# Kernel tuning notes

Measured on AMD Instinct MI355X. Metric: run time of the kernel, lower is better.

Reference implementation:

```python
import jax, jax.numpy as jnp
import numpy as np

B, N, RIN, ROUT, DEMB, FIN, FE, E, ITERS = 64, 128, 32, 64, 64, 64, 16, 65536, 3
NTOT = B * N


def gnn(x, edge_index, edge_feat, Ws, Wm, We, b):
    # edge-conditioned message passing: [NTOT, Fin] -> [NTOT, Fout]
    src, dst = edge_index[0], edge_index[1]
    msg = jax.nn.relu(x[src] @ Wm + edge_feat @ We)          # [E, Fout]
    agg = jax.ops.segment_sum(msg, dst, num_segments=x.shape[0])
    return jax.nn.relu(x @ Ws + agg + b)


def setup_inputs() -> dict:
    key = jax.random.key(0)
    ks = jax.random.split(key, 20)
    s = 0.1
    return {
        "x_r": jax.random.normal(ks[0], (NTOT, FIN), jnp.float32),
        "edge_index_r": jax.random.randint(ks[1], (2, E), 0, NTOT),
        "edge_feat_r": jax.random.normal(ks[2], (E, FE), jnp.float32),
        "x_p": jax.random.normal(ks[3], (NTOT, FIN), jnp.float32),
        "edge_index_p": jax.random.randint(ks[4], (2, E), 0, NTOT),
        "edge_feat_p": jax.random.normal(ks[5], (E, FE), jnp.float32),
        "r_mask": jnp.ones((B, N), dtype=bool),
        "p_mask": jnp.ones((B, N), dtype=bool),
        # gnn_1 params (FIN -> DEMB)
        "g1_Ws": jax.random.normal(ks[6], (FIN, DEMB)) * s,
        "g1_Wm": jax.random.normal(ks[7], (FIN, DEMB)) * s,
        "g1_We": jax.random.normal(ks[8], (FE, DEMB)) * s,
        "g1_b": jnp.zeros((DEMB,), jnp.float32),
        # gnn_2 params (RIN -> ROUT)
        "g2_Ws": jax.random.normal(ks[9], (RIN, ROUT)) * s,
        "g2_Wm": jax.random.normal(ks[10], (RIN, ROUT)) * s,
        "g2_We": jax.random.normal(ks[11], (FE, ROUT)) * s,
        "g2_b": jnp.zeros((ROUT,), jnp.float32),
        # consensus mlp (ROUT -> ROUT -> 1)
        "mlp_W1": jax.random.normal(ks[12], (ROUT, ROUT)) * s,
        "mlp_b1": jnp.zeros((ROUT,), jnp.float32),
        "mlp_W2": jax.random.normal(ks[13], (ROUT, 1)) * s,
        "mlp_b2": jnp.zeros((1,), jnp.float32),
    }


def reference(x_r, edge_index_r, edge_feat_r, x_p, edge_index_p, edge_feat_p,
              r_mask, p_mask,
              g1_Ws, g1_Wm, g1_We, g1_b,
              g2_Ws, g2_Wm, g2_We, g2_b,
              mlp_W1, mlp_b1, mlp_W2, mlp_b2):
    # node embeddings via gnn_1, then dense-batch to [B, N, DEMB]
    h_r = gnn(x_r, edge_index_r, edge_feat_r, g1_Ws, g1_Wm, g1_We, g1_b).reshape(B, N, DEMB)
    h_p = gnn(x_p, edge_index_p, edge_feat_p, g1_Ws, g1_Wm, g1_We, g1_b).reshape(B, N, DEMB)

    M_hat = jnp.einsum('brd,bpd->brp', h_r, h_p)             # [B, N_r, N_p]
    M_mask = r_mask[:, :, None] & p_mask[:, None, :]
    M_0 = jax.nn.softmax(M_hat, axis=-1).reshape(NTOT, N)    # packed (full mask)

    rkey = jax.random.key(42)
    for it in range(ITERS):
        M = jax.nn.softmax(M_hat, axis=-1)
        rf_r = jax.random.normal(jax.random.fold_in(rkey, it), (B, N, RIN), jnp.float32)
        rf_p = jnp.einsum('brp,bri->bpi', M, rf_r)           # M^T @ rand
        o_r = gnn(rf_r.reshape(NTOT, RIN), edge_index_r, edge_feat_r,
                  g2_Ws, g2_Wm, g2_We, g2_b).reshape(B, N, ROUT)
        o_p = gnn(rf_p.reshape(NTOT, RIN), edge_index_p, edge_feat_p,
                  g2_Ws, g2_Wm, g2_We, g2_b).reshape(B, N, ROUT)
        D = o_r[:, :, None, :] - o_p[:, None, :, :]          # [B, N_r, N_p, ROUT]
        upd = (jax.nn.relu(D @ mlp_W1 + mlp_b1) @ mlp_W2 + mlp_b2)[..., 0]
        M_hat = M_hat + jnp.where(M_mask, upd, 0.0)

    M_T = jax.nn.softmax(M_hat, axis=-1).reshape(NTOT, N)
    return (M_0, M_T)
```

## Files before the change

### kernel.cpp

```cpp
#include <hip/hip_runtime.h>

constexpr int kE = 65536, kNTOT = 8192;

__host__ __device__ __forceinline__ void tf_round(unsigned& x0, unsigned& x1, int r) {
  x0 += x1;
  x1 = (x1 << r) | (x1 >> (32 - r));
  x1 ^= x0;
}
__host__ __device__ __forceinline__ void tf2x32(unsigned k0, unsigned k1,
                                                unsigned& x0, unsigned& x1) {
  unsigned ks2 = k0 ^ k1 ^ 0x1BD11BDAu;
  x0 += k0; x1 += k1;
  tf_round(x0,x1,13); tf_round(x0,x1,15); tf_round(x0,x1,26); tf_round(x0,x1,6);
  x0 += k1; x1 += ks2 + 1u;
  tf_round(x0,x1,17); tf_round(x0,x1,29); tf_round(x0,x1,16); tf_round(x0,x1,24);
  x0 += ks2; x1 += k0 + 2u;
  tf_round(x0,x1,13); tf_round(x0,x1,15); tf_round(x0,x1,26); tf_round(x0,x1,6);
  x0 += k0; x1 += k1 + 3u;
  tf_round(x0,x1,17); tf_round(x0,x1,29); tf_round(x0,x1,16); tf_round(x0,x1,24);
  x0 += k1; x1 += ks2 + 4u;
  tf_round(x0,x1,13); tf_round(x0,x1,15); tf_round(x0,x1,26); tf_round(x0,x1,6);
  x0 += ks2; x1 += k0 + 5u;
}

__device__ __forceinline__ float bits_to_normal(unsigned bits) {
  float f = __uint_as_float((bits >> 9) | 0x3f800000u) - 1.0f;
  const float LO = -0.99999994f;
  float u = fmaf(f, 2.0f, LO);
  u = fmaxf(u, LO);
  float w = -log1pf(-u * u);
  float p;
  if (w < 5.0f) {
    w -= 2.5f;
    p = 2.81022636e-08f;
    p = fmaf(p, w, 3.43273939e-07f);
    p = fmaf(p, w, -3.5233877e-06f);
    p = fmaf(p, w, -4.39150654e-06f);
    p = fmaf(p, w, 0.00021858087f);
    p = fmaf(p, w, -0.00125372503f);
    p = fmaf(p, w, -0.00417768164f);
    p = fmaf(p, w, 0.246640727f);
    p = fmaf(p, w, 1.50140941f);
  } else {
    w = sqrtf(w) - 3.0f;
    p = -0.000200214257f;
    p = fmaf(p, w, 0.000100950558f);
    p = fmaf(p, w, 0.00134934322f);
    p = fmaf(p, w, -0.00367342844f);
    p = fmaf(p, w, 0.00573950773f);
    p = fmaf(p, w, -0.0076224613f);
    p = fmaf(p, w, 0.00943887047f);
    p = fmaf(p, w, 1.00167406f);
    p = fmaf(p, w, 2.83297682f);
  }
  return 1.41421356f * (p * u);
}

__device__ __forceinline__ float redmax32(float v) {
#pragma unroll
  for (int o = 16; o > 0; o >>= 1) v = fmaxf(v, __shfl_xor(v, o));
  return v;
}
__device__ __forceinline__ float redsum32(float v) {
#pragma unroll
  for (int o = 16; o > 0; o >>= 1) v += __shfl_xor(v, o);
  return v;
}

__global__ __launch_bounds__(256) void hist_kern(const int* __restrict__ eiR,
                                                 const int* __restrict__ eiP,
                                                 int* __restrict__ cntR,
                                                 int* __restrict__ cntP,
                                                 float* __restrict__ aggz) {
  int i = blockIdx.x * 256 + threadIdx.x;
  float4 z4 = make_float4(0.f, 0.f, 0.f, 0.f);
  float4* z = reinterpret_cast<float4*>(aggz) + i * 2;
  z[0] = z4; z[1] = z4;
  const int* ei = (i < kE) ? eiR : eiP;
  int* cnt = (i < kE) ? cntR : cntP;
  int e = i & (kE - 1);
  atomicAdd(&cnt[ei[kE + e]], 1);
}

__global__ __launch_bounds__(256) void scan_kern(const int* __restrict__ cntR,
                                                 int* __restrict__ rpR, int* __restrict__ offR,
                                                 const int* __restrict__ cntP,
                                                 int* __restrict__ rpP, int* __restrict__ offP) {
  const int* cnt = blockIdx.x ? cntP : cntR;
  int* rp = blockIdx.x ? rpP : rpR;
  int* off = blockIdx.x ? offP : offR;
  int t = threadIdx.x;
  int base = t * 32;
  int v[32];
#pragma unroll
  for (int i = 0; i < 32; ++i) v[i] = cnt[base + i];
  int sum = 0;
#pragma unroll
  for (int i = 0; i < 32; ++i) sum += v[i];
  int lane = t & 63, w = t >> 6;
  int incl = sum;
#pragma unroll
  for (int o = 1; o < 64; o <<= 1) {
    int y = __shfl_up(incl, o);
    if (lane >= o) incl += y;
  }
  __shared__ int wsum[4];
  if (lane == 63) wsum[w] = incl;
  __syncthreads();
  int woff = 0;
#pragma unroll
  for (int i = 0; i < 4; ++i) if (i < w) woff += wsum[i];
  int running = woff + incl - sum;
#pragma unroll
  for (int i = 0; i < 32; ++i) {
    rp[base + i] = running;
    off[base + i] = running;
    running += v[i];
  }
  if (t == 0) rp[kNTOT] = kE;
}

__global__ __launch_bounds__(256) void scatter_kern(
    const int* __restrict__ eiR, const int* __restrict__ eiP,
    int* __restrict__ offR, int* __restrict__ offP,
    int* __restrict__ permR, int* __restrict__ permP,
    int* __restrict__ srcsR, int* __restrict__ srcsP,
    int* __restrict__ dstsR, int* __restrict__ dstsP) {
  int i = blockIdx.x * 256 + threadIdx.x;
  const int* ei = (i < kE) ? eiR : eiP;
  int* off = (i < kE) ? offR : offP;
  int* perm = (i < kE) ? permR : permP;
  int* srcs = (i < kE) ? srcsR : srcsP;
  int* dsts = (i < kE) ? dstsR : dstsP;
  int e = i & (kE - 1);
  int dst = ei[kE + e];
  int pos = atomicAdd(&off[dst], 1);
  perm[pos] = e;
  srcs[pos] = ei[e];
  dsts[pos] = dst;
}

template <int KX>
__global__ __launch_bounds__(256) void msg_gemm(
    const float* __restrict__ xR, const float* __restrict__ efR,
    const int* __restrict__ srcsR, const int* __restrict__ permR,
    const int* __restrict__ dstsR, float* __restrict__ aggR,
    const float* __restrict__ xP, const float* __restrict__ efP,
    const int* __restrict__ srcsP, const int* __restrict__ permP,
    const int* __restrict__ dstsP, float* __restrict__ aggP,
    const float* __restrict__ Wm, const float* __restrict__ We) {
  constexpr int KT = KX + 16;
  constexpr int SA_ROWS = (KT > 64) ? KT : 64;
  __shared__ float sA[SA_ROWS][68];
  __shared__ float sW[KT][68];
  __shared__ int sDst[64];
  bool isP = blockIdx.x >= 1024;
  const float* x = isP ? xP : xR;
  const float* ef = isP ? efP : efR;
  const int* srcs = isP ? srcsP : srcsR;
  const int* perm = isP ? permP : permR;
  const int* dsts = isP ? dstsP : dstsR;
  float* agg = isP ? aggP : aggR;
  int i0 = (blockIdx.x & 1023) * 64;
  int t = threadIdx.x;
#pragma unroll
  for (int idx = 0; idx < KT * 64 / 1024; ++idx) {
    int q = t * 4 + idx * 1024;
    int k = q >> 6, j = q & 63;
    const float* sp = (k < KX) ? (Wm + k * 64 + j) : (We + (k - KX) * 64 + j);
    float4 v = *reinterpret_cast<const float4*>(sp);
    *reinterpret_cast<float4*>(&sW[k][j]) = v;
  }
  if (t < 64) sDst[t] = dsts[i0 + t];
#pragma unroll
  for (int idx = 0; idx < KT * 64 / 1024; ++idx) {
    int q = t * 4 + idx * 1024;
    int r = q / KT;
    int k = q % KT;
    const float* rptr = (k < KX) ? (x + (size_t)srcs[i0 + r] * KX + k)
                                 : (ef + (size_t)perm[i0 + r] * 16 + (k - KX));
    float4 v = *reinterpret_cast<const float4*>(rptr);
    sA[k + 0][r] = v.x; sA[k + 1][r] = v.y; sA[k + 2][r] = v.z; sA[k + 3][r] = v.w;
  }
  __syncthreads();
  int tn = (t & 15) * 4;
  int tj = (t >> 4) * 4;
  float acc[4][4] = {};
#pragma unroll 8
  for (int k = 0; k < KT; ++k) {
    float4 a = *reinterpret_cast<const float4*>(&sA[k][tn]);
    float4 b = *reinterpret_cast<const float4*>(&sW[k][tj]);
    acc[0][0] = fmaf(a.x, b.x, acc[0][0]); acc[0][1] = fmaf(a.x, b.y, acc[0][1]);
    acc[0][2] = fmaf(a.x, b.z, acc[0][2]); acc[0][3] = fmaf(a.x, b.w, acc[0][3]);
    acc[1][0] = fmaf(a.y, b.x, acc[1][0]); acc[1][1] = fmaf(a.y, b.y, acc[1][1]);
    acc[1][2] = fmaf(a.y, b.z, acc[1][2]); acc[1][3] = fmaf(a.y, b.w, acc[1][3]);
    acc[2][0] = fmaf(a.z, b.x, acc[2][0]); acc[2][1] = fmaf(a.z, b.y, acc[2][1]);
    acc[2][2] = fmaf(a.z, b.z, acc[2][2]); acc[2][3] = fmaf(a.z, b.w, acc[2][3]);
    acc[3][0] = fmaf(a.w, b.x, acc[3][0]); acc[3][1] = fmaf(a.w, b.y, acc[3][1]);
    acc[3][2] = fmaf(a.w, b.z, acc[3][2]); acc[3][3] = fmaf(a.w, b.w, acc[3][3]);
  }
  __syncthreads();
#pragma unroll
  for (int i = 0; i < 4; ++i) {
    sA[tn + i][tj + 0] = fmaxf(acc[i][0], 0.f);
    sA[tn + i][tj + 1] = fmaxf(acc[i][1], 0.f);
    sA[tn + i][tj + 2] = fmaxf(acc[i][2], 0.f);
    sA[tn + i][tj + 3] = fmaxf(acc[i][3], 0.f);
  }
  __syncthreads();
  int col = t & 63;
  int r0l = (t >> 6) * 16;
  float run = 0.f;
  int rd = sDst[r0l];
#pragma unroll
  for (int r = 0; r < 16; ++r) {
    int d = sDst[r0l + r];
    if (d != rd) {
      unsafeAtomicAdd(&agg[(size_t)rd * 64 + col], run);
      run = 0.f; rd = d;
    }
    run += sA[r0l + r][col];
  }
  unsafeAtomicAdd(&agg[(size_t)rd * 64 + col], run);
}

__global__ __launch_bounds__(256) void node1_gemm(
    const float* __restrict__ xR, float* __restrict__ aggR, float* __restrict__ hR,
    const float* __restrict__ xP, float* __restrict__ aggP, float* __restrict__ hP,
    const float* __restrict__ Ws, const float* __restrict__ bias) {
  __shared__ float sX[64][68];
  __shared__ float sW[64][68];
  bool isP = blockIdx.x >= 128;
  const float* x = isP ? xP : xR;
  float* agg = isP ? aggP : aggR;
  float* h = isP ? hP : hR;
  int n0 = (blockIdx.x & 127) * 64;
  int t = threadIdx.x;
#pragma unroll
  for (int idx = 0; idx < 4; ++idx) {
    int q = t * 4 + idx * 1024;
    int k = q >> 6, j = q & 63;
    *reinterpret_cast<float4*>(&sW[k][j]) = *reinterpret_cast<const float4*>(Ws + q);
    float4 v = *reinterpret_cast<const float4*>(x + (size_t)n0 * 64 + q);
    sX[j + 0][k] = v.x; sX[j + 1][k] = v.y; sX[j + 2][k] = v.z; sX[j + 3][k] = v.w;
  }
  __syncthreads();
  int tn = (t & 15) * 4, tj = (t >> 4) * 4;
  float acc[4][4] = {};
#pragma unroll 8
  for (int k = 0; k < 64; ++k) {
    float4 a = *reinterpret_cast<const float4*>(&sX[k][tn]);
    float4 b = *reinterpret_cast<const float4*>(&sW[k][tj]);
    acc[0][0] = fmaf(a.x, b.x, acc[0][0]); acc[0][1] = fmaf(a.x, b.y, acc[0][1]);
    acc[0][2] = fmaf(a.x, b.z, acc[0][2]); acc[0][3] = fmaf(a.x, b.w, acc[0][3]);
    acc[1][0] = fmaf(a.y, b.x, acc[1][0]); acc[1][1] = fmaf(a.y, b.y, acc[1][1]);
    acc[1][2] = fmaf(a.y, b.z, acc[1][2]); acc[1][3] = fmaf(a.y, b.w, acc[1][3]);
    acc[2][0] = fmaf(a.z, b.x, acc[2][0]); acc[2][1] = fmaf(a.z, b.y, acc[2][1]);
    acc[2][2] = fmaf(a.z, b.z, acc[2][2]); acc[2][3] = fmaf(a.z, b.w, acc[2][3]);
    acc[3][0] = fmaf(a.w, b.x, acc[3][0]); acc[3][1] = fmaf(a.w, b.y, acc[3][1]);
    acc[3][2] = fmaf(a.w, b.z, acc[3][2]); acc[3][3] = fmaf(a.w, b.w, acc[3][3]);
  }
  float4 bv = *reinterpret_cast<const float4*>(bias + tj);
  float4 z4 = make_float4(0.f, 0.f, 0.f, 0.f);
#pragma unroll
  for (int i = 0; i < 4; ++i) {
    int n = n0 + tn + i;
    float4 g = *reinterpret_cast<const float4*>(&agg[(size_t)n * 64 + tj]);
    *reinterpret_cast<float4*>(&agg[(size_t)n * 64 + tj]) = z4;
    float4 o;
    o.x = fmaxf(acc[i][0] + g.x + bv.x, 0.f);
    o.y = fmaxf(acc[i][1] + g.y + bv.y, 0.f);
    o.z = fmaxf(acc[i][2] + g.z + bv.z, 0.f);
    o.w = fmaxf(acc[i][3] + g.w + bv.w, 0.f);
    *reinterpret_cast<float4*>(&h[(size_t)n * 64 + tj]) = o;
  }
}

__global__ __launch_bounds__(256) void mhat_soft(
    const float* __restrict__ hR, const float* __restrict__ hP,
    float* __restrict__ Mhat, float* __restrict__ Msoft, float* __restrict__ M0out,
    float* __restrict__ rfr, unsigned fk0, unsigned fk1) {
  __shared__ float hr[16][66];
  __shared__ float hp[128][66];
  int gid = blockIdx.x, t = threadIdx.x;
  int gtid = (gid << 8) + t;
#pragma unroll
  for (int q = 0; q < 2; ++q) {
    unsigned i = (unsigned)gtid + (unsigned)q * 131072u;
    unsigned a0 = 0u, a1 = i;
    tf2x32(fk0, fk1, a0, a1);
    rfr[i] = bits_to_normal(a0 ^ a1);
  }
  int b = gid >> 3, r0 = (gid & 7) * 16;
  const float* hrG = hR + ((size_t)(b * 128 + r0)) * 64;
  {
    int q = t * 4; int r = q >> 6, d = q & 63;
    float4 v = *reinterpret_cast<const float4*>(hrG + q);
    hr[r][d] = v.x; hr[r][d + 1] = v.y; hr[r][d + 2] = v.z; hr[r][d + 3] = v.w;
  }
  const float* hpG = hP + (size_t)b * 128 * 64;
#pragma unroll
  for (int rep = 0; rep < 8; ++rep) {
    int q = (rep * 256 + t) * 4; int p = q >> 6, d = q & 63;
    float4 v = *reinterpret_cast<const float4*>(hpG + q);
    hp[p][d] = v.x; hp[p][d + 1] = v.y; hp[p][d + 2] = v.z; hp[p][d + 3] = v.w;
  }
  __syncthreads();
  int tx = t & 31, ty = t >> 5;
  float acc[2][4] = {};
  for (int d = 0; d < 64; ++d) {
    float a0 = hr[ty][d], a1 = hr[ty + 8][d];
    float q0 = hp[tx][d], q1 = hp[tx + 32][d], q2 = hp[tx + 64][d], q3 = hp[tx + 96][d];
    acc[0][0] = fmaf(a0, q0, acc[0][0]); acc[0][1] = fmaf(a0, q1, acc[0][1]);
    acc[0][2] = fmaf(a0, q2, acc[0][2]); acc[0][3] = fmaf(a0, q3, acc[0][3]);
    acc[1][0] = fmaf(a1, q0, acc[1][0]); acc[1][1] = fmaf(a1, q1, acc[1][1]);
    acc[1][2] = fmaf(a1, q2, acc[1][2]); acc[1][3] = fmaf(a1, q3, acc[1][3]);
  }
#pragma unroll
  for (int ii = 0; ii < 2; ++ii) {
    int r = r0 + ty + 8 * ii;
    float* mrow = Mhat + ((size_t)(b * 128 + r)) * 128;
    mrow[tx] = acc[ii][0]; mrow[tx + 32] = acc[ii][1];
    mrow[tx + 64] = acc[ii][2]; mrow[tx + 96] = acc[ii][3];
    float mx = redmax32(fmaxf(fmaxf(acc[ii][0], acc[ii][1]), fmaxf(acc[ii][2], acc[ii][3])));
    float e0 = __expf(acc[ii][0] - mx), e1 = __expf(acc[ii][1] - mx);
    float e2 = __expf(acc[ii][2] - mx), e3 = __expf(acc[ii][3] - mx);
    float inv = 1.0f / redsum32(e0 + e1 + e2 + e3);
    float* srow = Msoft + ((size_t)(b * 128 + r)) * 128;
    srow[tx] = e0 * inv; srow[tx + 32] = e1 * inv;
    srow[tx + 64] = e2 * inv; srow[tx + 96] = e3 * inv;
    float* orow = M0out + ((size_t)(b * 128 + r)) * 128;
    orow[tx] = e0 * inv; orow[tx + 32] = e1 * inv;
    orow[tx + 64] = e2 * inv; orow[tx + 96] = e3 * inv;
  }
}

__global__ __launch_bounds__(256) void rfp_kern(
    const float* __restrict__ Msoft, const float* __restrict__ rfr,
    float* __restrict__ rfp) {
  __shared__ float rr[128][36];
  int b = blockIdx.x >> 3, p0 = (blockIdx.x & 7) * 16;
  int t = threadIdx.x;
  const float* rfG = rfr + (size_t)b * 4096;
#pragma unroll
  for (int rep = 0; rep < 4; ++rep) {
    int q = (rep * 256 + t) * 4; int r = q >> 5, i = q & 31;
    float4 v = *reinterpret_cast<const float4*>(rfG + q);
    rr[r][i] = v.x; rr[r][i + 1] = v.y; rr[r][i + 2] = v.z; rr[r][i + 3] = v.w;
  }
  __syncthreads();
  int pl = t & 15, ih = (t >> 4) * 2;
  int p = p0 + pl;
  const float* Mcol = Msoft + (size_t)b * 16384 + p;
  float a0 = 0.f, a1 = 0.f;
#pragma unroll 8
  for (int r = 0; r < 128; ++r) {
    float m = Mcol[(size_t)r * 128];
    a0 = fmaf(m, rr[r][ih], a0);
    a1 = fmaf(m, rr[r][ih + 1], a1);
  }
  float* dst = rfp + ((size_t)(b * 128 + p)) * 32 + ih;
  dst[0] = a0; dst[1] = a1;
}

__global__ __launch_bounds__(256) void node2u_gemm(
    const float* __restrict__ rfR, float* __restrict__ aggR, float* __restrict__ uR,
    const float* __restrict__ rfP, float* __restrict__ aggP, float* __restrict__ uP,
    const float* __restrict__ Ws2, const float* __restrict__ g2b,
    const float* __restrict__ W1, const float* __restrict__ b1) {
  __shared__ float sRF[32][68];
  __shared__ float sW2[32][68];
  __shared__ float sW1[64][68];
  __shared__ float sO[64][68];
  bool isP = blockIdx.x >= 128;
  const float* rf = isP ? rfP : rfR;
  float* agg = isP ? aggP : aggR;
  float* u = isP ? uP : uR;
  int n0 = (blockIdx.x & 127) * 64;
  int t = threadIdx.x;
#pragma unroll
  for (int idx = 0; idx < 4; ++idx) {
    int q = t * 4 + idx * 1024;
    *reinterpret_cast<float4*>(&sW1[q >> 6][q & 63]) = *reinterpret_cast<const float4*>(W1 + q);
  }
#pragma unroll
  for (int idx = 0; idx < 2; ++idx) {
    int q = t * 4 + idx * 1024;
    *reinterpret_cast<float4*>(&sW2[q >> 6][q & 63]) = *reinterpret_cast<const float4*>(Ws2 + q);
    int r = q >> 5, kk = q & 31;
    float4 v = *reinterpret_cast<const float4*>(rf + (size_t)(n0 + r) * 32 + kk);
    sRF[kk][r] = v.x; sRF[kk + 1][r] = v.y; sRF[kk + 2][r] = v.z; sRF[kk + 3][r] = v.w;
  }
  __syncthreads();
  int tn = (t & 15) * 4, tj = (t >> 4) * 4;
  float acc[4][4] = {};
#pragma unroll 8
  for (int k = 0; k < 32; ++k) {
    float4 a = *reinterpret_cast<const float4*>(&sRF[k][tn]);
    float4 b = *reinterpret_cast<const float4*>(&sW2[k][tj]);
    acc[0][0] = fmaf(a.x, b.x, acc[0][0]); acc[0][1] = fmaf(a.x, b.y, acc[0][1]);
    acc[0][2] = fmaf(a.x, b.z, acc[0][2]); acc[0][3] = fmaf(a.x, b.w, acc[0][3]);
    acc[1][0] = fmaf(a.y, b.x, acc[1][0]); acc[1][1] = fmaf(a.y, b.y, acc[1][1]);
    acc[1][2] = fmaf(a.y, b.z, acc[1][2]); acc[1][3] = fmaf(a.y, b.w, acc[1][3]);
    acc[2][0] = fmaf(a.z, b.x, acc[2][0]); acc[2][1] = fmaf(a.z, b.y, acc[2][1]);
    acc[2][2] = fmaf(a.z, b.z, acc[2][2]); acc[2][3] = fmaf(a.z, b.w, acc[2][3]);
    acc[3][0] = fmaf(a.w, b.x, acc[3][0]); acc[3][1] = fmaf(a.w, b.y, acc[3][1]);
    acc[3][2] = fmaf(a.w, b.z, acc[3][2]); acc[3][3] = fmaf(a.w, b.w, acc[3][3]);
  }
  float4 bg = *reinterpret_cast<const float4*>(g2b + tj);
  float4 z4 = make_float4(0.f, 0.f, 0.f, 0.f);
#pragma unroll
  for (int i = 0; i < 4; ++i) {
    int n = n0 + tn + i;
    float4 g = *reinterpret_cast<const float4*>(&agg[(size_t)n * 64 + tj]);
    *reinterpret_cast<float4*>(&agg[(size_t)n * 64 + tj]) = z4;
    sO[tj + 0][tn + i] = fmaxf(acc[i][0] + g.x + bg.x, 0.f);
    sO[tj + 1][tn + i] = fmaxf(acc[i][1] + g.y + bg.y, 0.f);
    sO[tj + 2][tn + i] = fmaxf(acc[i][2] + g.z + bg.z, 0.f);
    sO[tj + 3][tn + i] = fmaxf(acc[i][3] + g.w + bg.w, 0.f);
  }
  __syncthreads();
  float acc2[4][4] = {};
#pragma unroll 8
  for (int k = 0; k < 64; ++k) {
    float4 a = *reinterpret_cast<const float4*>(&sO[k][tn]);
    float4 b = *reinterpret_cast<const float4*>(&sW1[k][tj]);
    acc2[0][0] = fmaf(a.x, b.x, acc2[0][0]); acc2[0][1] = fmaf(a.x, b.y, acc2[0][1]);
    acc2[0][2] = fmaf(a.x, b.z, acc2[0][2]); acc2[0][3] = fmaf(a.x, b.w, acc2[0][3]);
    acc2[1][0] = fmaf(a.y, b.x, acc2[1][0]); acc2[1][1] = fmaf(a.y, b.y, acc2[1][1]);
    acc2[1][2] = fmaf(a.y, b.z, acc2[1][2]); acc2[1][3] = fmaf(a.y, b.w, acc2[1][3]);
    acc2[2][0] = fmaf(a.z, b.x, acc2[2][0]); acc2[2][1] = fmaf(a.z, b.y, acc2[2][1]);
    acc2[2][2] = fmaf(a.z, b.z, acc2[2][2]); acc2[2][3] = fmaf(a.z, b.w, acc2[2][3]);
    acc2[3][0] = fmaf(a.w, b.x, acc2[3][0]); acc2[3][1] = fmaf(a.w, b.y, acc2[3][1]);
    acc2[3][2] = fmaf(a.w, b.z, acc2[3][2]); acc2[3][3] = fmaf(a.w, b.w, acc2[3][3]);
  }
  float4 b1v = make_float4(0.f, 0.f, 0.f, 0.f);
  if (!isP) b1v = *reinterpret_cast<const float4*>(b1 + tj);
#pragma unroll
  for (int i = 0; i < 4; ++i) {
    int n = n0 + tn + i;
    float4 o;
    o.x = acc2[i][0] + b1v.x; o.y = acc2[i][1] + b1v.y;
    o.z = acc2[i][2] + b1v.z; o.w = acc2[i][3] + b1v.w;
    *reinterpret_cast<float4*>(&u[(size_t)n * 64 + tj]) = o;
  }
}

__global__ __launch_bounds__(256) void upd_soft(
    const float* __restrict__ uR, const float* __restrict__ uP,
    const float* __restrict__ W2, const float* __restrict__ b2p,
    float* __restrict__ Mhat, float* __restrict__ softDst,
    int writeMhat, float* __restrict__ rfr, int doRng,
    unsigned fk0, unsigned fk1) {
  __shared__ float sur[16][66];
  __shared__ float sup[128][66];
  __shared__ float sw2[64];
  int gid = blockIdx.x, t = threadIdx.x;
  int b = gid >> 3, r0 = (gid & 7) * 16;
  const float* urG = uR + ((size_t)(b * 128 + r0)) * 64;
  {
    int q = t * 4; int r = q >> 6, d = q & 63;
    float4 v = *reinterpret_cast<const float4*>(urG + q);
    sur[r][d] = v.x; sur[r][d + 1] = v.y; sur[r][d + 2] = v.z; sur[r][d + 3] = v.w;
  }
  const float* upG = uP + (size_t)b * 128 * 64;
#pragma unroll
  for (int rep = 0; rep < 8; ++rep) {
    int q = (rep * 256 + t) * 4; int p = q >> 6, d = q & 63;
    float4 v = *reinterpret_cast<const float4*>(upG + q);
    sup[p][d] = v.x; sup[p][d + 1] = v.y; sup[p][d + 2] = v.z; sup[p][d + 3] = v.w;
  }
  if (t < 64) sw2[t] = W2[t];
  __syncthreads();
  int tx = t & 31, ty = t >> 5;
  float acc[2][4] = {};
  for (int j = 0; j < 64; ++j) {
    float w2v = sw2[j];
    float a0 = sur[ty][j], a1 = sur[ty + 8][j];
    float q0 = sup[tx][j], q1 = sup[tx + 32][j], q2 = sup[tx + 64][j], q3 = sup[tx + 96][j];
    acc[0][0] = fmaf(fmaxf(a0 - q0, 0.f), w2v, acc[0][0]);
    acc[0][1] = fmaf(fmaxf(a0 - q1, 0.f), w2v, acc[0][1]);
    acc[0][2] = fmaf(fmaxf(a0 - q2, 0.f), w2v, acc[0][2]);
    acc[0][3] = fmaf(fmaxf(a0 - q3, 0.f), w2v, acc[0][3]);
    acc[1][0] = fmaf(fmaxf(a1 - q0, 0.f), w2v, acc[1][0]);
    acc[1][1] = fmaf(fmaxf(a1 - q1, 0.f), w2v, acc[1][1]);
    acc[1][2] = fmaf(fmaxf(a1 - q2, 0.f), w2v, acc[1][2]);
    acc[1][3] = fmaf(fmaxf(a1 - q3, 0.f), w2v, acc[1][3]);
  }
  float b2v = b2p[0];
#pragma unroll
  for (int ii = 0; ii < 2; ++ii) {
    int r = r0 + ty + 8 * ii;
    float* mrow = Mhat + ((size_t)(b * 128 + r)) * 128;
    float m0 = mrow[tx] + acc[ii][0] + b2v;
    float m1 = mrow[tx + 32] + acc[ii][1] + b2v;
    float m2 = mrow[tx + 64] + acc[ii][2] + b2v;
    float m3 = mrow[tx + 96] + acc[ii][3] + b2v;
    if (writeMhat) {
      mrow[tx] = m0; mrow[tx + 32] = m1; mrow[tx + 64] = m2; mrow[tx + 96] = m3;
    }
    float mx = redmax32(fmaxf(fmaxf(m0, m1), fmaxf(m2, m3)));
    float e0 = __expf(m0 - mx), e1 = __expf(m1 - mx);
    float e2 = __expf(m2 - mx), e3 = __expf(m3 - mx);
    float inv = 1.0f / redsum32(e0 + e1 + e2 + e3);
    float* srow = softDst + ((size_t)(b * 128 + r)) * 128;
    srow[tx] = e0 * inv; srow[tx + 32] = e1 * inv;
    srow[tx + 64] = e2 * inv; srow[tx + 96] = e3 * inv;
  }
  if (doRng) {
    int gtid = (gid << 8) + t;
#pragma unroll
    for (int q = 0; q < 2; ++q) {
      unsigned i = (unsigned)gtid + (unsigned)q * 131072u;
      unsigned a0 = 0u, a1 = i;
      tf2x32(fk0, fk1, a0, a1);
      rfr[i] = bits_to_normal(a0 ^ a1);
    }
  }
}

extern "C" void kernel_launch(void* const* d_in, const int* in_sizes, int n_in,
                              void* d_out, int out_size, void* d_ws, size_t ws_size,
                              hipStream_t stream) {
  (void)in_sizes; (void)n_in; (void)out_size; (void)ws_size;
  const float* x_r  = (const float*)d_in[0];
  const int*   ei_r = (const int*)d_in[1];
  const float* ef_r = (const float*)d_in[2];
  const float* x_p  = (const float*)d_in[3];
  const int*   ei_p = (const int*)d_in[4];
  const float* ef_p = (const float*)d_in[5];
  const float* g1_Ws = (const float*)d_in[8];
  const float* g1_Wm = (const float*)d_in[9];
  const float* g1_We = (const float*)d_in[10];
  const float* g1_b  = (const float*)d_in[11];
  const float* g2_Ws = (const float*)d_in[12];
  const float* g2_Wm = (const float*)d_in[13];
  const float* g2_We = (const float*)d_in[14];
  const float* g2_b  = (const float*)d_in[15];
  const float* W1 = (const float*)d_in[16];
  const float* b1 = (const float*)d_in[17];
  const float* W2 = (const float*)d_in[18];
  const float* b2 = (const float*)d_in[19];
  float* out = (float*)d_out;

  float* ws = (float*)d_ws;
  float* h_r   = ws;
  float* h_p   = h_r + 524288;
  float* Mhat  = h_p + 524288;
  float* Msoft = Mhat + 1048576;
  float* rfr   = Msoft + 1048576;
  float* rfp   = rfr + 262144;
  float* u_r   = rfp + 262144;
  float* u_p   = u_r + 524288;
  float* agg_r = u_p + 524288;
  float* agg_p = agg_r + 524288;
  int* ib      = (int*)(agg_p + 524288);
  int* cnt_r  = ib;
  int* cnt_p  = cnt_r + 8192;
  int* off_r  = cnt_p + 8192;
  int* off_p  = off_r + 8192;
  int* rp_r   = off_p + 8192;
  int* rp_p   = rp_r + 8193;
  int* perm_r = rp_p + 8193;
  int* perm_p = perm_r + 65536;
  int* srcs_r = perm_p + 65536;
  int* srcs_p = srcs_r + 65536;
  int* dsts_r = srcs_p + 65536;
  int* dsts_p = dsts_r + 65536;

  unsigned fk0[3], fk1[3];
  for (int it = 0; it < 3; ++it) {
    unsigned a = 0u, c = (unsigned)it;
    tf2x32(0u, 42u, a, c);
    fk0[it] = a; fk1[it] = c;
  }

  hipMemsetAsync(cnt_r, 0, 2 * 8192 * sizeof(int), stream);
  hist_kern<<<512, 256, 0, stream>>>(ei_r, ei_p, cnt_r, cnt_p, agg_r);
  scan_kern<<<2, 256, 0, stream>>>(cnt_r, rp_r, off_r, cnt_p, rp_p, off_p);
  scatter_kern<<<512, 256, 0, stream>>>(ei_r, ei_p, off_r, off_p,
                                        perm_r, perm_p, srcs_r, srcs_p,
                                        dsts_r, dsts_p);

  msg_gemm<64><<<2048, 256, 0, stream>>>(x_r, ef_r, srcs_r, perm_r, dsts_r, agg_r,
                                         x_p, ef_p, srcs_p, perm_p, dsts_p, agg_p,
                                         g1_Wm, g1_We);
  node1_gemm<<<256, 256, 0, stream>>>(x_r, agg_r, h_r, x_p, agg_p, h_p, g1_Ws, g1_b);
  mhat_soft<<<512, 256, 0, stream>>>(h_r, h_p, Mhat, Msoft, out, rfr, fk0[0], fk1[0]);

  for (int it = 0; it < 3; ++it) {
    rfp_kern<<<512, 256, 0, stream>>>(Msoft, rfr, rfp);
    msg_gemm<32><<<2048, 256, 0, stream>>>(rfr, ef_r, srcs_r, perm_r, dsts_r, agg_r,
                                           rfp, ef_p, srcs_p, perm_p, dsts_p, agg_p,
                                           g2_Wm, g2_We);
    node2u_gemm<<<256, 256, 0, stream>>>(rfr, agg_r, u_r, rfp, agg_p, u_p,
                                         g2_Ws, g2_b, W1, b1);
    int last = (it == 2);
    upd_soft<<<512, 256, 0, stream>>>(u_r, u_p, W2, b2, Mhat,
                                      last ? (out + 1048576) : Msoft,
                                      !last,
                                      rfr, !last,
                                      fk0[it < 2 ? it + 1 : 0], fk1[it < 2 ? it + 1 : 0]);
  }
}
```

Measured before the change: 316.6 us.

## Precompute edge-feature projections once and split gnn_2 message GEMM into node-level products

The loop-invariant edge-feature product ef@We for gnn_2 is computed once, as extra blocks of the first message kernel, and stored per sorted edge. Each iteration then computes x@Wm at node level (8192 rows instead of 65536 edges), fused into the rfp kernel, and a lightweight gather-add-relu kernel builds the messages and does the segmented atomic aggregation. This removes the per-edge GEMM work from the loop. In exchange it adds 32 MB of workspace for the per-edge projections, which must be streamed from memory every iteration. The unused cnt/rp buffers are also dropped from the scan.

Result: no change. 320.2 us (+1.1%).

```diff
diff --git a/kernel.cpp b/kernel.cpp
--- a/kernel.cpp
+++ b/kernel.cpp
@@ -69,31 +69,27 @@
 
 __global__ __launch_bounds__(256) void hist_kern(const int* __restrict__ eiR,
                                                  const int* __restrict__ eiP,
-                                                 int* __restrict__ cntR,
-                                                 int* __restrict__ cntP,
+                                                 int* __restrict__ offR,
+                                                 int* __restrict__ offP,
                                                  float* __restrict__ aggz) {
   int i = blockIdx.x * 256 + threadIdx.x;
   float4 z4 = make_float4(0.f, 0.f, 0.f, 0.f);
   float4* z = reinterpret_cast<float4*>(aggz) + i * 2;
   z[0] = z4; z[1] = z4;
   const int* ei = (i < kE) ? eiR : eiP;
-  int* cnt = (i < kE) ? cntR : cntP;
+  int* off = (i < kE) ? offR : offP;
   int e = i & (kE - 1);
-  atomicAdd(&cnt[ei[kE + e]], 1);
-}
-
-__global__ __launch_bounds__(256) void scan_kern(const int* __restrict__ cntR,
-                                                 int* __restrict__ rpR, int* __restrict__ offR,
-                                                 const int* __restrict__ cntP,
-                                                 int* __restrict__ rpP, int* __restrict__ offP) {
-  const int* cnt = blockIdx.x ? cntP : cntR;
-  int* rp = blockIdx.x ? rpP : rpR;
+  atomicAdd(&off[ei[kE + e]], 1);
+}
+
+__global__ __launch_bounds__(256) void scan_kern(int* __restrict__ offR,
+                                                 int* __restrict__ offP) {
   int* off = blockIdx.x ? offP : offR;
   int t = threadIdx.x;
   int base = t * 32;
   int v[32];
 #pragma unroll
-  for (int i = 0; i < 32; ++i) v[i] = cnt[base + i];
+  for (int i = 0; i < 32; ++i) v[i] = off[base + i];
   int sum = 0;
 #pragma unroll
   for (int i = 0; i < 32; ++i) sum += v[i];
@@ -113,11 +109,9 @@
   int running = woff + incl - sum;
 #pragma unroll
   for (int i = 0; i < 32; ++i) {
-    rp[base + i] = running;
     off[base + i] = running;
     running += v[i];
   }
-  if (t == 0) rp[kNTOT] = kE;
 }
 
 __global__ __launch_bounds__(256) void scatter_kern(
@@ -148,12 +142,55 @@
     const float* __restrict__ xP, const float* __restrict__ efP,
     const int* __restrict__ srcsP, const int* __restrict__ permP,
     const int* __restrict__ dstsP, float* __restrict__ aggP,
-    const float* __restrict__ Wm, const float* __restrict__ We) {
+    const float* __restrict__ Wm, const float* __restrict__ We,
+    const float* __restrict__ We2, float* __restrict__ efweR, float* __restrict__ efweP) {
   constexpr int KT = KX + 16;
   constexpr int SA_ROWS = (KT > 64) ? KT : 64;
   __shared__ float sA[SA_ROWS][68];
   __shared__ float sW[KT][68];
   __shared__ int sDst[64];
+  int t = threadIdx.x;
+  if (blockIdx.x >= 2048) {
+    int tile = blockIdx.x - 2048;
+    bool isP2 = tile >= 1024;
+    const float* ef2 = isP2 ? efP : efR;
+    const int* perm2 = isP2 ? permP : permR;
+    float* ew = isP2 ? efweP : efweR;
+    int i0 = (tile & 1023) * 64;
+    {
+      int q = t * 4;
+      int k = q >> 6, j = q & 63;
+      *reinterpret_cast<float4*>(&sW[k][j]) = *reinterpret_cast<const float4*>(We2 + q);
+    }
+    {
+      int q = t * 4;
+      int r = q >> 4, k = q & 15;
+      float4 v = *reinterpret_cast<const float4*>(ef2 + (size_t)perm2[i0 + r] * 16 + k);
+      sA[k + 0][r] = v.x; sA[k + 1][r] = v.y; sA[k + 2][r] = v.z; sA[k + 3][r] = v.w;
+    }
+    __syncthreads();
+    int tn = (t & 15) * 4, tj = (t >> 4) * 4;
+    float acc[4][4] = {};
+#pragma unroll
+    for (int k = 0; k < 16; ++k) {
+      float4 a = *reinterpret_cast<const float4*>(&sA[k][tn]);
+      float4 b = *reinterpret_cast<const float4*>(&sW[k][tj]);
+      acc[0][0] = fmaf(a.x, b.x, acc[0][0]); acc[0][1] = fmaf(a.x, b.y, acc[0][1]);
+      acc[0][2] = fmaf(a.x, b.z, acc[0][2]); acc[0][3] = fmaf(a.x, b.w, acc[0][3]);
+      acc[1][0] = fmaf(a.y, b.x, acc[1][0]); acc[1][1] = fmaf(a.y, b.y, acc[1][1]);
+      acc[1][2] = fmaf(a.y, b.z, acc[1][2]); acc[1][3] = fmaf(a.y, b.w, acc[1][3]);
+      acc[2][0] = fmaf(a.z, b.x, acc[2][0]); acc[2][1] = fmaf(a.z, b.y, acc[2][1]);
+      acc[2][2] = fmaf(a.z, b.z, acc[2][2]); acc[2][3] = fmaf(a.z, b.w, acc[2][3]);
+      acc[3][0] = fmaf(a.w, b.x, acc[3][0]); acc[3][1] = fmaf(a.w, b.y, acc[3][1]);
+      acc[3][2] = fmaf(a.w, b.z, acc[3][2]); acc[3][3] = fmaf(a.w, b.w, acc[3][3]);
+    }
+#pragma unroll
+    for (int i = 0; i < 4; ++i) {
+      float4 o = make_float4(acc[i][0], acc[i][1], acc[i][2], acc[i][3]);
+      *reinterpret_cast<float4*>(&ew[(size_t)(i0 + tn + i) * 64 + tj]) = o;
+    }
+    return;
+  }
   bool isP = blockIdx.x >= 1024;
   const float* x = isP ? xP : xR;
   const float* ef = isP ? efP : efR;
@@ -162,7 +199,6 @@
   const int* dsts = isP ? dstsP : dstsR;
   float* agg = isP ? aggP : aggR;
   int i0 = (blockIdx.x & 1023) * 64;
-  int t = threadIdx.x;
 #pragma unroll
   for (int idx = 0; idx < KT * 64 / 1024; ++idx) {
     int q = t * 4 + idx * 1024;
@@ -224,6 +260,36 @@
   unsafeAtomicAdd(&agg[(size_t)rd * 64 + col], run);
 }
 
+__global__ __launch_bounds__(256) void msg_add(
+    const float* __restrict__ xwmR, const float* __restrict__ efweR,
+    const int* __restrict__ srcsR, const int* __restrict__ dstsR, float* __restrict__ aggR,
+    const float* __restrict__ xwmP, const float* __restrict__ efweP,
+    const int* __restrict__ srcsP, const int* __restrict__ dstsP, float* __restrict__ aggP) {
+  int lane = threadIdx.x & 63;
+  int wv = blockIdx.x * 4 + (threadIdx.x >> 6);
+  bool isP = wv >= 4096;
+  const float* xwm = isP ? xwmP : xwmR;
+  const float* efwe = isP ? efweP : efweR;
+  const int* srcs = isP ? srcsP : srcsR;
+  const int* dsts = isP ? dstsP : dstsR;
+  float* agg = isP ? aggP : aggR;
+  int e0 = (wv & 4095) * 16;
+  float run = 0.f;
+  int rd = dsts[e0];
+#pragma unroll 4
+  for (int k = 0; k < 16; ++k) {
+    int e = e0 + k;
+    int d = dsts[e];
+    if (d != rd) {
+      unsafeAtomicAdd(&agg[(size_t)rd * 64 + lane], run);
+      run = 0.f; rd = d;
+    }
+    float v = xwm[(size_t)srcs[e] * 64 + lane] + efwe[(size_t)e * 64 + lane];
+    run += fmaxf(v, 0.f);
+  }
+  unsafeAtomicAdd(&agg[(size_t)rd * 64 + lane], run);
+}
+
 __global__ __launch_bounds__(256) void node1_gemm(
     const float* __restrict__ xR, float* __restrict__ aggR, float* __restrict__ hR,
     const float* __restrict__ xP, float* __restrict__ aggP, float* __restrict__ hP,
@@ -335,32 +401,88 @@
   }
 }
 
-__global__ __launch_bounds__(256) void rfp_kern(
+__global__ __launch_bounds__(256) void rfp_xwm_kern(
     const float* __restrict__ Msoft, const float* __restrict__ rfr,
-    float* __restrict__ rfp) {
-  __shared__ float rr[128][36];
-  int b = blockIdx.x >> 3, p0 = (blockIdx.x & 7) * 16;
+    float* __restrict__ rfp, const float* __restrict__ Wm2,
+    float* __restrict__ xwm_r, float* __restrict__ xwm_p) {
+  __shared__ __align__(16) float sm[7232];
   int t = threadIdx.x;
-  const float* rfG = rfr + (size_t)b * 4096;
-#pragma unroll
-  for (int rep = 0; rep < 4; ++rep) {
-    int q = (rep * 256 + t) * 4; int r = q >> 5, i = q & 31;
-    float4 v = *reinterpret_cast<const float4*>(rfG + q);
-    rr[r][i] = v.x; rr[r][i + 1] = v.y; rr[r][i + 2] = v.z; rr[r][i + 3] = v.w;
-  }
-  __syncthreads();
-  int pl = t & 15, ih = (t >> 4) * 2;
-  int p = p0 + pl;
-  const float* Mcol = Msoft + (size_t)b * 16384 + p;
-  float a0 = 0.f, a1 = 0.f;
+  if (blockIdx.x < 512) {
+    float (*rr)[36] = (float(*)[36])sm;
+    float (*srow)[36] = (float(*)[36])(sm + 4608);
+    float (*swm)[64] = (float(*)[64])(sm + 5184);
+    int b = blockIdx.x >> 3, p0 = (blockIdx.x & 7) * 16;
+    const float* rfG = rfr + (size_t)b * 4096;
+#pragma unroll
+    for (int rep = 0; rep < 4; ++rep) {
+      int q = (rep * 256 + t) * 4; int r = q >> 5, i = q & 31;
+      float4 v = *reinterpret_cast<const float4*>(rfG + q);
+      rr[r][i] = v.x; rr[r][i + 1] = v.y; rr[r][i + 2] = v.z; rr[r][i + 3] = v.w;
+    }
+#pragma unroll
+    for (int rep = 0; rep < 2; ++rep) {
+      int q = t * 4 + rep * 1024;
+      *reinterpret_cast<float4*>(&swm[q >> 6][q & 63]) = *reinterpret_cast<const float4*>(Wm2 + q);
+    }
+    __syncthreads();
+    int pl = t & 15, ih = (t >> 4) * 2;
+    int p = p0 + pl;
+    const float* Mcol = Msoft + (size_t)b * 16384 + p;
+    float a0 = 0.f, a1 = 0.f;
 #pragma unroll 8
-  for (int r = 0; r < 128; ++r) {
-    float m = Mcol[(size_t)r * 128];
-    a0 = fmaf(m, rr[r][ih], a0);
-    a1 = fmaf(m, rr[r][ih + 1], a1);
-  }
-  float* dst = rfp + ((size_t)(b * 128 + p)) * 32 + ih;
-  dst[0] = a0; dst[1] = a1;
+    for (int r = 0; r < 128; ++r) {
+      float m = Mcol[(size_t)r * 128];
+      a0 = fmaf(m, rr[r][ih], a0);
+      a1 = fmaf(m, rr[r][ih + 1], a1);
+    }
+    float* dst = rfp + ((size_t)(b * 128 + p)) * 32 + ih;
+    dst[0] = a0; dst[1] = a1;
+    srow[pl][ih] = a0; srow[pl][ih + 1] = a1;
+    __syncthreads();
+    int r2 = t & 15, c2 = (t >> 4) * 4;
+    float4 av = make_float4(0.f, 0.f, 0.f, 0.f);
+#pragma unroll 8
+    for (int k = 0; k < 32; ++k) {
+      float s = srow[r2][k];
+      float4 w = *reinterpret_cast<const float4*>(&swm[k][c2]);
+      av.x = fmaf(s, w.x, av.x); av.y = fmaf(s, w.y, av.y);
+      av.z = fmaf(s, w.z, av.z); av.w = fmaf(s, w.w, av.w);
+    }
+    *reinterpret_cast<float4*>(&xwm_p[(size_t)(b * 128 + p0 + r2) * 64 + c2]) = av;
+  } else {
+    float (*sRF)[68] = (float(*)[68])sm;
+    float (*swm)[64] = (float(*)[64])(sm + 2176);
+    int n0 = (blockIdx.x - 512) * 64;
+#pragma unroll
+    for (int rep = 0; rep < 2; ++rep) {
+      int q = t * 4 + rep * 1024;
+      *reinterpret_cast<float4*>(&swm[q >> 6][q & 63]) = *reinterpret_cast<const float4*>(Wm2 + q);
+      int r = q >> 5, kk = q & 31;
+      float4 v = *reinterpret_cast<const float4*>(rfr + (size_t)(n0 + r) * 32 + kk);
+      sRF[kk][r] = v.x; sRF[kk + 1][r] = v.y; sRF[kk + 2][r] = v.z; sRF[kk + 3][r] = v.w;
+    }
+    __syncthreads();
+    int tn = (t & 15) * 4, tj = (t >> 4) * 4;
+    float acc[4][4] = {};
+#pragma unroll 8
+    for (int k = 0; k < 32; ++k) {
+      float4 a = *reinterpret_cast<const float4*>(&sRF[k][tn]);
+      float4 b = *reinterpret_cast<const float4*>(&swm[k][tj]);
+      acc[0][0] = fmaf(a.x, b.x, acc[0][0]); acc[0][1] = fmaf(a.x, b.y, acc[0][1]);
+      acc[0][2] = fmaf(a.x, b.z, acc[0][2]); acc[0][3] = fmaf(a.x, b.w, acc[0][3]);
+      acc[1][0] = fmaf(a.y, b.x, acc[1][0]); acc[1][1] = fmaf(a.y, b.y, acc[1][1]);
+      acc[1][2] = fmaf(a.y, b.z, acc[1][2]); acc[1][3] = fmaf(a.y, b.w, acc[1][3]);
+      acc[2][0] = fmaf(a.z, b.x, acc[2][0]); acc[2][1] = fmaf(a.z, b.y, acc[2][1]);
+      acc[2][2] = fmaf(a.z, b.z, acc[2][2]); acc[2][3] = fmaf(a.z, b.w, acc[2][3]);
+      acc[3][0] = fmaf(a.w, b.x, acc[3][0]); acc[3][1] = fmaf(a.w, b.y, acc[3][1]);
+      acc[3][2] = fmaf(a.w, b.z, acc[3][2]); acc[3][3] = fmaf(a.w, b.w, acc[3][3]);
+    }
+#pragma unroll
+    for (int i = 0; i < 4; ++i) {
+      float4 o = make_float4(acc[i][0], acc[i][1], acc[i][2], acc[i][3]);
+      *reinterpret_cast<float4*>(&xwm_r[(size_t)(n0 + tn + i) * 64 + tj]) = o;
+    }
+  }
 }
 
 __global__ __launch_bounds__(256) void node2u_gemm(
@@ -554,19 +676,19 @@
   float* u_p   = u_r + 524288;
   float* agg_r = u_p + 524288;
   float* agg_p = agg_r + 524288;
-  int* ib      = (int*)(agg_p + 524288);
-  int* cnt_r  = ib;
-  int* cnt_p  = cnt_r + 8192;
-  int* off_r  = cnt_p + 8192;
+  float* efwe_r = agg_p + 524288;
+  float* efwe_p = efwe_r + 4194304;
+  int* ib      = (int*)(efwe_p + 4194304);
+  int* off_r  = ib;
   int* off_p  = off_r + 8192;
-  int* rp_r   = off_p + 8192;
-  int* rp_p   = rp_r + 8193;
-  int* perm_r = rp_p + 8193;
+  int* perm_r = off_p + 8192;
   int* perm_p = perm_r + 65536;
   int* srcs_r = perm_p + 65536;
   int* srcs_p = srcs_r + 65536;
   int* dsts_r = srcs_p + 65536;
   int* dsts_p = dsts_r + 65536;
+  float* xwm_r = u_r;
+  float* xwm_p = u_p;
 
   unsigned fk0[3], fk1[3];
   for (int it = 0; it < 3; ++it) {
@@ -575,24 +697,23 @@
     fk0[it] = a; fk1[it] = c;
   }
 
-  hipMemsetAsync(cnt_r, 0, 2 * 8192 * sizeof(int), stream);
-  hist_kern<<<512, 256, 0, stream>>>(ei_r, ei_p, cnt_r, cnt_p, agg_r);
-  scan_kern<<<2, 256, 0, stream>>>(cnt_r, rp_r, off_r, cnt_p, rp_p, off_p);
+  hipMemsetAsync(off_r, 0, 2 * 8192 * sizeof(int), stream);
+  hist_kern<<<512, 256, 0, stream>>>(ei_r, ei_p, off_r, off_p, agg_r);
+  scan_kern<<<2, 256, 0, stream>>>(off_r, off_p);
   scatter_kern<<<512, 256, 0, stream>>>(ei_r, ei_p, off_r, off_p,
                                         perm_r, perm_p, srcs_r, srcs_p,
                                         dsts_r, dsts_p);
 
-  msg_gemm<64><<<2048, 256, 0, stream>>>(x_r, ef_r, srcs_r, perm_r, dsts_r, agg_r,
+  msg_gemm<64><<<4096, 256, 0, stream>>>(x_r, ef_r, srcs_r, perm_r, dsts_r, agg_r,
                                          x_p, ef_p, srcs_p, perm_p, dsts_p, agg_p,
-                                         g1_Wm, g1_We);
+                                         g1_Wm, g1_We, g2_We, efwe_r, efwe_p);
   node1_gemm<<<256, 256, 0, stream>>>(x_r, agg_r, h_r, x_p, agg_p, h_p, g1_Ws, g1_b);
   mhat_soft<<<512, 256, 0, stream>>>(h_r, h_p, Mhat, Msoft, out, rfr, fk0[0], fk1[0]);
 
   for (int it = 0; it < 3; ++it) {
-    rfp_kern<<<512, 256, 0, stream>>>(Msoft, rfr, rfp);
-    msg_gemm<32><<<2048, 256, 0, stream>>>(rfr, ef_r, srcs_r, perm_r, dsts_r, agg_r,
-                                           rfp, ef_p, srcs_p, perm_p, dsts_p, agg_p,
-                                           g2_Wm, g2_We);
+    rfp_xwm_kern<<<640, 256, 0, stream>>>(Msoft, rfr, rfp, g2_Wm, xwm_r, xwm_p);
+    msg_add<<<2048, 256, 0, stream>>>(xwm_r, efwe_r, srcs_r, dsts_r, agg_r,
+                                      xwm_p, efwe_p, srcs_p, dsts_p, agg_p);
     node2u_gemm<<<256, 256, 0, stream>>>(rfr, agg_r, u_r, rfp, agg_p, u_p,
                                          g2_Ws, g2_b, W1, b1);
     int last = (it == 2);
```
